# Performance work log

Hardware: AMD Instinct MI355X
Metric: run time of the kernel (lower is better)

Reference implementation:

```python
import jax, jax.numpy as jnp
import numpy as np

WIN = (7, 7)
N_TOK = WIN[0] * WIN[1]          # 49
DIM = 512
HEADS = 16
B_WIN = 2048                     # num_windows * batch
NW = 64                          # windows per image (mask leading dim)


def _relative_position_index():
    # Mirrors the torch __init__ coords computation.
    coords = np.stack(np.meshgrid(np.arange(WIN[0]), np.arange(WIN[1]), indexing='ij'))  # [2,Wh,Ww]
    flat = coords.reshape(2, -1)                                   # [2, N]
    rel = flat[:, :, None] - flat[:, None, :]                      # [2, N, N]
    rel = rel.transpose(1, 2, 0).astype(np.int32)                  # [N, N, 2]
    rel[:, :, 0] += WIN[0] - 1
    rel[:, :, 1] += WIN[1] - 1
    rel[:, :, 0] *= 2 * WIN[1] - 1
    return jnp.asarray(rel.sum(-1), dtype=jnp.int32)               # [N, N]


def setup_inputs() -> dict:
    key = jax.random.key(0)
    ks = jax.random.split(key, 7)
    x = jax.random.normal(ks[0], (B_WIN, N_TOK, DIM), jnp.float32)
    w_qkv = jax.random.normal(ks[1], (3 * DIM, DIM), jnp.float32) * 0.02
    b_qkv = jax.random.normal(ks[2], (3 * DIM,), jnp.float32) * 0.02
    w_proj = jax.random.normal(ks[3], (DIM, DIM), jnp.float32) * 0.02
    b_proj = jax.random.normal(ks[4], (DIM,), jnp.float32) * 0.02
    bias_table = jax.random.normal(ks[5], ((2 * WIN[0] - 1) * (2 * WIN[1] - 1), HEADS), jnp.float32) * 0.02
    rel_index = _relative_position_index()
    # shift-window mask: 0 for allowed, -100 for masked (Swin convention)
    mask = jnp.where(jax.random.bernoulli(ks[6], 0.1, (NW, N_TOK, N_TOK)), -100.0, 0.0).astype(jnp.float32)
    return {"x": x, "w_qkv": w_qkv, "b_qkv": b_qkv, "w_proj": w_proj,
            "b_proj": b_proj, "bias_table": bias_table, "rel_index": rel_index, "mask": mask}


def reference(x, w_qkv, b_qkv, w_proj, b_proj, bias_table, rel_index, mask):
    B_, N, C = x.shape
    H = HEADS
    hd = C // H
    scale = hd ** -0.5
    # qkv projection: [B, N, 3, H, hd] -> q,k,v each [B, H, N, hd]
    qkv = (jnp.einsum('bnc,oc->bno', x, w_qkv) + b_qkv)
    qkv = qkv.reshape(B_, N, 3, H, hd).transpose(2, 0, 3, 1, 4)
    q, k, v = qkv[0], qkv[1], qkv[2]
    attn = jnp.einsum('bhnd,bhmd->bhnm', q * scale, k)             # [B, H, N, N]
    # relative position bias gather: [N*N] -> [N, N, H] -> [H, N, N]
    rpb = bias_table[rel_index.reshape(-1)].reshape(N, N, H).transpose(2, 0, 1)
    attn = attn + rpb[None]
    nW = mask.shape[0]
    attn = attn.reshape(B_ // nW, nW, H, N, N) + mask[None, :, None]
    attn = attn.reshape(B_, H, N, N)
    attn = jax.nn.softmax(attn, axis=-1)
    out = jnp.einsum('bhnm,bhmd->bhnd', attn, v)                   # [B, H, N, hd]
    out = out.transpose(0, 2, 1, 3).reshape(B_, N, C)
    out = jnp.einsum('bnc,oc->bno', out, w_proj) + b_proj
    return out
```

## Files before the change

### kernel.cpp

```cpp
#include <hip/hip_runtime.h>
#include <stdint.h>

typedef unsigned short u16;
typedef unsigned int u32;
typedef unsigned long long u64;
typedef __attribute__((ext_vector_type(4))) u16 u16x4;
typedef __attribute__((ext_vector_type(8))) u16 u16x8;
typedef __attribute__((ext_vector_type(2))) u32 u32x2;
typedef __attribute__((ext_vector_type(8))) short bf16x8;
typedef __attribute__((ext_vector_type(4))) float f32x4;

#define DEVFN __device__ __forceinline__

DEVFN u16 f2bf(float f) {
  union { float f; u32 u; } x; x.f = f;
  u32 u = x.u;
  return (u16)((u + 0x7fffu + ((u >> 16) & 1u)) >> 16);
}
DEVFN float bf2f(u16 v) {
  union { u32 u; float f; } x; x.u = ((u32)v) << 16;
  return x.f;
}

__global__ void cvt_kernel(const float* __restrict__ in, u16* __restrict__ out, int n4) {
  const int stride = gridDim.x * blockDim.x;
  for (int i = blockIdx.x * blockDim.x + threadIdx.x; i < n4; i += stride) {
    float4 v = reinterpret_cast<const float4*>(in)[i];
    u16x4 o;
    o.x = f2bf(v.x); o.y = f2bf(v.y); o.z = f2bf(v.z); o.w = f2bf(v.w);
    reinterpret_cast<u16x4*>(out)[i] = o;
  }
}

__global__ void pbb_kernel(const float* __restrict__ bt, const int* __restrict__ ri,
                           u16* __restrict__ pbb) {
  const int h = blockIdx.x;
  for (int t = threadIdx.x; t < 4096; t += 256) {
    const int i = t >> 6, j = t & 63;
    float v = 0.f;
    if (i < 49 && j < 49) v = bt[ri[i * 49 + j] * 16 + h];
    pbb[h * 4096 + t] = f2bf(v);
  }
}

__global__ void mbits_kernel(const float* __restrict__ mask, u64* __restrict__ mb) {
  const int w = blockIdx.x;
  const int i = threadIdx.x;
  u64 m = ~0ull << 49;
  if (i < 49) {
    for (int j = 0; j < 49; ++j)
      if (mask[w * 2401 + i * 49 + j] < -1.0f) m |= 1ull << j;
  } else {
    m = ~0ull;
  }
  mb[w * 64 + i] = m;
}

#define WAIT_LGKM0 asm volatile("s_waitcnt lgkmcnt(0)" ::: "memory")
#define WAIT_LGKM8 asm volatile("s_waitcnt lgkmcnt(8)" ::: "memory")
#define WAIT_VM2   asm volatile("s_waitcnt vmcnt(2)" ::: "memory")
#define WAIT_VM0   asm volatile("s_waitcnt vmcnt(0)" ::: "memory")
#define SCHEDB     __builtin_amdgcn_sched_barrier(0)
#define BARRIER    __builtin_amdgcn_s_barrier()
#define MFMA(a, b, c) __builtin_amdgcn_mfma_f32_16x16x32_bf16(a, b, c, 0, 0, 0)

template <int MODE, int NTILES, int MCHUNK>
__global__ __launch_bounds__(512) void gemm_kernel(
    const u16* __restrict__ A, const u16* __restrict__ Bt,
    const float* __restrict__ bias, void* __restrict__ Out, int ldo) {
  extern __shared__ u16 smem[];
  const int tid = threadIdx.x;
  const int lane = tid & 63;
  const int wid = tid >> 6;
  const int bid = blockIdx.x;
  const int xcd = bid & 7;
  const int slot = bid >> 3;
  const int m0 = (xcd * MCHUNK + slot / NTILES) * 256;
  const int n0 = (slot % NTILES) * 256;
  const int wr = wid >> 2, wc = wid & 3;
  const int l15 = lane & 15, lg = lane >> 4;
  const int rg0 = tid >> 3;
  const int sl0 = tid & 7;

  f32x4 acc[8][4] = {};

#define STAGE_RAW(kt_, hp_)                                                    \
  {                                                                            \
    const u16* srcp_ = ((hp_) < 2)                                             \
        ? (A + (size_t)(m0 + ((hp_) & 1) * 128) * 512)                         \
        : (Bt + (size_t)(n0 + ((hp_) & 1) * 128) * 512);                       \
    u16* dst_ = smem + ((kt_) & 1) * 32768 + (hp_) * 8192;                     \
    _Pragma("unroll") for (int i_ = 0; i_ < 2; ++i_) {                         \
      const int rg_ = i_ * 64 + rg0;                                           \
      const int kc_ = sl0 ^ (rg_ & 7);                                         \
      const u16* g_ = srcp_ + (size_t)rg_ * 512 + (kt_) * 64 + kc_ * 8;        \
      __builtin_amdgcn_global_load_lds(                                        \
          (const __attribute__((address_space(1))) void*)g_,                   \
          (__attribute__((address_space(3))) void*)(dst_ + i_ * 4096 + wid * 512), \
          16, 0, 0);                                                           \
    }                                                                          \
  }

#define STG(g_)                                                                \
  if ((g_) >= 3 && (g_) < 27) {                                                \
    const int s_ = (g_) - 3;                                                   \
    STAGE_RAW(2 + s_ / 4, s_ & 3);                                             \
  }

#define RDA(dst, mi_, ks_)                                                     \
  {                                                                            \
    const int row_ = wr * 128 + (mi_) * 16 + l15;                              \
    dst = *reinterpret_cast<const bf16x8*>(                                    \
        smem + cb + row_ * 64 + ((((ks_) * 4 + lg) ^ (row_ & 7)) << 3));       \
  }
#define RDB(dst, ni_, ks_)                                                     \
  {                                                                            \
    const int row_ = wc * 64 + (ni_) * 16 + l15;                               \
    dst = *reinterpret_cast<const bf16x8*>(                                    \
        smem + cb + 16384 + row_ * 64 + ((((ks_) * 4 + lg) ^ (row_ & 7)) << 3)); \
  }

#pragma unroll
  for (int hp = 0; hp < 4; ++hp) STAGE_RAW(0, hp);
#pragma unroll
  for (int hp = 0; hp < 4; ++hp) STAGE_RAW(1, hp);
  WAIT_VM0; SCHEDB;
  BARRIER; SCHEDB;

#pragma unroll
  for (int kt = 0; kt < 8; ++kt) {
    const int cb = (kt & 1) * 32768;
    const int g0 = kt * 4;
    bf16x8 a0[4][2], a1[4][2], b0[2][2], b1[2][2];

#pragma unroll
    for (int mi = 0; mi < 4; ++mi) { RDA(a0[mi][0], mi, 0); RDA(a0[mi][1], mi, 1); }
#pragma unroll
    for (int ni = 0; ni < 2; ++ni) { RDB(b0[ni][0], ni, 0); RDB(b0[ni][1], ni, 1); }
    STG(g0 + 0);
    WAIT_LGKM8; SCHEDB;
    BARRIER;
    WAIT_LGKM0; SCHEDB;
    __builtin_amdgcn_s_setprio(1);
#pragma unroll
    for (int mi = 0; mi < 4; ++mi)
#pragma unroll
      for (int ni = 0; ni < 2; ++ni)
#pragma unroll
        for (int ks = 0; ks < 2; ++ks)
          acc[mi][ni] = MFMA(a0[mi][ks], b0[ni][ks], acc[mi][ni]);
    __builtin_amdgcn_s_setprio(0); SCHEDB;
    BARRIER; SCHEDB;

#pragma unroll
    for (int ni = 0; ni < 2; ++ni) { RDB(b1[ni][0], ni + 2, 0); RDB(b1[ni][1], ni + 2, 1); }
    STG(g0 + 1);
    BARRIER;
    WAIT_LGKM0; SCHEDB;
    __builtin_amdgcn_s_setprio(1);
#pragma unroll
    for (int mi = 0; mi < 4; ++mi)
#pragma unroll
      for (int ni = 0; ni < 2; ++ni)
#pragma unroll
        for (int ks = 0; ks < 2; ++ks)
          acc[mi][ni + 2] = MFMA(a0[mi][ks], b1[ni][ks], acc[mi][ni + 2]);
    __builtin_amdgcn_s_setprio(0); SCHEDB;
    BARRIER; SCHEDB;

#pragma unroll
    for (int mi = 0; mi < 4; ++mi) { RDA(a1[mi][0], mi + 4, 0); RDA(a1[mi][1], mi + 4, 1); }
    STG(g0 + 2);
    BARRIER;
    WAIT_LGKM0; SCHEDB;
    __builtin_amdgcn_s_setprio(1);
#pragma unroll
    for (int mi = 0; mi < 4; ++mi)
#pragma unroll
      for (int ni = 0; ni < 2; ++ni)
#pragma unroll
        for (int ks = 0; ks < 2; ++ks)
          acc[mi + 4][ni + 2] = MFMA(a1[mi][ks], b1[ni][ks], acc[mi + 4][ni + 2]);
    __builtin_amdgcn_s_setprio(0); SCHEDB;
    BARRIER; SCHEDB;

    STG(g0 + 3);
    BARRIER; SCHEDB;
    __builtin_amdgcn_s_setprio(1);
#pragma unroll
    for (int mi = 0; mi < 4; ++mi)
#pragma unroll
      for (int ni = 0; ni < 2; ++ni)
#pragma unroll
        for (int ks = 0; ks < 2; ++ks)
          acc[mi + 4][ni] = MFMA(a1[mi][ks], b0[ni][ks], acc[mi + 4][ni]);
    __builtin_amdgcn_s_setprio(0); SCHEDB;
    if (g0 + 3 == 27) { WAIT_VM0; }
    else if (g0 + 3 < 27) { WAIT_VM2; }
    SCHEDB;
    BARRIER; SCHEDB;
  }
#undef STAGE_RAW
#undef STG
#undef RDA
#undef RDB

#pragma unroll
  for (int mi = 0; mi < 8; ++mi) {
#pragma unroll
    for (int ni = 0; ni < 4; ++ni) {
      const int col = n0 + wc * 64 + ni * 16 + l15;
      const float bv = bias[col];
      const int rbase = m0 + wr * 128 + mi * 16 + lg * 4;
#pragma unroll
      for (int r = 0; r < 4; ++r) {
        const float v = acc[mi][ni][r] + bv;
        if (MODE == 0) {
          ((u16*)Out)[(size_t)(rbase + r) * ldo + col] = f2bf(v);
        } else {
          ((float*)Out)[(size_t)(rbase + r) * ldo + col] = v;
        }
      }
    }
  }
}

__global__ __launch_bounds__(256) void attn_kernel(
    const u16* __restrict__ qkv, const u16* __restrict__ pbb,
    const u64* __restrict__ mbits, u16* __restrict__ attn_out) {
  const int w = threadIdx.x >> 6;
  const int lane = threadIdx.x & 63;
  const int b = blockIdx.x >> 2;
  const int h = ((blockIdx.x & 3) << 2) | w;
  const int l15 = lane & 15, lg = lane >> 4;
  const int lg4 = lg * 4;

  __shared__ u16 sVT[4][32][72];
  u16 (*vt)[72] = sVT[w];

  for (int i = lane; i < 1152; i += 64) ((u32*)vt)[i] = 0;

  const size_t rowbase = (size_t)b * (49 * 1536) + h * 32;

  for (int c = lane; c < 196; c += 64) {
    const int n = c >> 2, dg = c & 3;
    u16x8 vv = *reinterpret_cast<const u16x8*>(qkv + rowbase + (size_t)n * 1536 + 1024 + dg * 8);
    const int pin = ((n >> 5) << 5) | ((((n >> 2) & 3)) << 3) | (((n >> 4) & 1) << 2) | (n & 3);
#pragma unroll
    for (int j = 0; j < 8; ++j) vt[dg * 8 + j][pin] = vv[j];
  }

  bf16x8 aq[4], bk[4];
#pragma unroll
  for (int t = 0; t < 4; ++t) {
    const int i = t * 16 + l15;
    const int r = i < 49 ? i : 48;
    const size_t ro = rowbase + (size_t)r * 1536 + lg * 8;
    aq[t] = *reinterpret_cast<const bf16x8*>(qkv + ro);
    bk[t] = *reinterpret_cast<const bf16x8*>(qkv + ro + 512);
  }

  const u64* mwb = mbits + ((b & 63) << 6);
  u64 mb[4];
#pragma unroll
  for (int qt = 0; qt < 4; ++qt) mb[qt] = mwb[qt * 16 + l15];

  bf16x8 bv[2][2];
#pragma unroll
  for (int ni = 0; ni < 2; ++ni)
#pragma unroll
    for (int ks = 0; ks < 2; ++ks)
      bv[ni][ks] = *reinterpret_cast<const bf16x8*>(&vt[ni * 16 + l15][ks * 32 + lg * 8]);

  const float scale = 0.17677669529663687f;
  const u16* pbh = pbb + (h << 12);
  const size_t obase = (size_t)b * 49 * 512 + h * 32;

#pragma unroll
  for (int qt = 0; qt < 4; ++qt) {
    f32x4 sT[4] = {};
#pragma unroll
    for (int kt = 0; kt < 4; ++kt)
      sT[kt] = __builtin_amdgcn_mfma_f32_16x16x32_bf16(bk[kt], aq[qt], sT[kt], 0, 0, 0);

    const int i = qt * 16 + l15;
    const u16* pr = pbh + i * 64 + lg4;
    float v[4][4];
    float mx = -3e38f;
#pragma unroll
    for (int kt = 0; kt < 4; ++kt) {
      u16x4 pv = *reinterpret_cast<const u16x4*>(pr + kt * 16);
      const u32 nib = (u32)(mb[qt] >> (kt * 16 + lg4)) & 0xFu;
#pragma unroll
      for (int r = 0; r < 4; ++r) {
        float val = fmaf(sT[kt][r], scale, bf2f(pv[r]));
        if (nib & (1u << r)) val -= 100.f;
        if (kt == 3 && (lg4 + r) >= 1) val = -1e30f;
        v[kt][r] = val;
        mx = fmaxf(mx, val);
      }
    }
    mx = fmaxf(mx, __shfl_xor(mx, 16));
    mx = fmaxf(mx, __shfl_xor(mx, 32));
    float sum = 0.f;
#pragma unroll
    for (int kt = 0; kt < 4; ++kt)
#pragma unroll
      for (int r = 0; r < 4; ++r) {
        const float e = __expf(v[kt][r] - mx);
        v[kt][r] = e;
        sum += e;
      }
    sum += __shfl_xor(sum, 16);
    sum += __shfl_xor(sum, 32);
    const float rinv = 1.0f / sum;

    bf16x8 ap[2];
#pragma unroll
    for (int ks = 0; ks < 2; ++ks) {
      u32 w0 = (u32)f2bf(v[2 * ks][0] * rinv) | ((u32)f2bf(v[2 * ks][1] * rinv) << 16);
      u32 w1 = (u32)f2bf(v[2 * ks][2] * rinv) | ((u32)f2bf(v[2 * ks][3] * rinv) << 16);
      u32 w2 = (u32)f2bf(v[2 * ks + 1][0] * rinv) | ((u32)f2bf(v[2 * ks + 1][1] * rinv) << 16);
      u32 w3 = (u32)f2bf(v[2 * ks + 1][2] * rinv) | ((u32)f2bf(v[2 * ks + 1][3] * rinv) << 16);
      union { u32 u[4]; bf16x8 b; } pk;
      pk.u[0] = w0; pk.u[1] = w1; pk.u[2] = w2; pk.u[3] = w3;
      ap[ks] = pk.b;
    }

    f32x4 o[2] = {};
#pragma unroll
    for (int ks = 0; ks < 2; ++ks)
#pragma unroll
      for (int ni = 0; ni < 2; ++ni)
        o[ni] = __builtin_amdgcn_mfma_f32_16x16x32_bf16(ap[ks], bv[ni][ks], o[ni], 0, 0, 0);

#pragma unroll
    for (int r = 0; r < 4; ++r) {
      const int iq = qt * 16 + lg4 + r;
      if (iq < 49) {
#pragma unroll
        for (int ni = 0; ni < 2; ++ni)
          attn_out[obase + (size_t)iq * 512 + ni * 16 + l15] = f2bf(o[ni][r]);
      }
    }
  }
}

extern "C" void kernel_launch(void* const* d_in, const int* in_sizes, int n_in,
                              void* d_out, int out_size, void* d_ws, size_t ws_size,
                              hipStream_t stream) {
  (void)in_sizes; (void)n_in; (void)out_size; (void)ws_size;
  const float* x          = (const float*)d_in[0];
  const float* w_qkv      = (const float*)d_in[1];
  const float* b_qkv      = (const float*)d_in[2];
  const float* w_proj     = (const float*)d_in[3];
  const float* b_proj     = (const float*)d_in[4];
  const float* bias_table = (const float*)d_in[5];
  const int*   rel_index  = (const int*)d_in[6];
  const float* mask       = (const float*)d_in[7];

  u16* ws     = (u16*)d_ws;
  u16* xbf    = ws;
  u16* qkv    = ws + 51380224;
  u16* wqkvb  = qkv + 154140672;
  u16* wprojb = wqkvb + 786432;
  u16* pbb    = wprojb + 262144;
  u64* mbits  = (u64*)(pbb + 65536);

  (void)hipFuncSetAttribute((const void*)gemm_kernel<0, 6, 49>,
                            hipFuncAttributeMaxDynamicSharedMemorySize, 131072);
  (void)hipFuncSetAttribute((const void*)gemm_kernel<1, 2, 49>,
                            hipFuncAttributeMaxDynamicSharedMemorySize, 131072);

  cvt_kernel<<<2048, 256, 0, stream>>>(x, xbf, 51380224 / 4);
  cvt_kernel<<<192, 256, 0, stream>>>(w_qkv, wqkvb, 786432 / 4);
  cvt_kernel<<<64, 256, 0, stream>>>(w_proj, wprojb, 262144 / 4);
  pbb_kernel<<<16, 256, 0, stream>>>(bias_table, rel_index, pbb);
  mbits_kernel<<<64, 64, 0, stream>>>(mask, mbits);

  gemm_kernel<0, 6, 49><<<2352, 512, 131072, stream>>>(xbf, wqkvb, b_qkv, qkv, 1536);
  attn_kernel<<<8192, 256, 0, stream>>>(qkv, pbb, mbits, xbf);
  gemm_kernel<1, 2, 49><<<784, 512, 131072, stream>>>(xbf, wprojb, b_proj, d_out, 512);
}
```

Baseline: 505.4 us.

## Reschedule GEMM prefetch stages, use nontemporal stores, and XCD-swizzle attention blocks

```diff
diff --git a/kernel.cpp b/kernel.cpp
--- a/kernel.cpp
+++ b/kernel.cpp
@@ -58,7 +58,7 @@
 
 #define WAIT_LGKM0 asm volatile("s_waitcnt lgkmcnt(0)" ::: "memory")
 #define WAIT_LGKM8 asm volatile("s_waitcnt lgkmcnt(8)" ::: "memory")
-#define WAIT_VM2   asm volatile("s_waitcnt vmcnt(2)" ::: "memory")
+#define WAIT_VM4   asm volatile("s_waitcnt vmcnt(4)" ::: "memory")
 #define WAIT_VM0   asm volatile("s_waitcnt vmcnt(0)" ::: "memory")
 #define SCHEDB     __builtin_amdgcn_sched_barrier(0)
 #define BARRIER    __builtin_amdgcn_s_barrier()
@@ -101,12 +101,6 @@
     }                                                                          \
   }
 
-#define STG(g_)                                                                \
-  if ((g_) >= 3 && (g_) < 27) {                                                \
-    const int s_ = (g_) - 3;                                                   \
-    STAGE_RAW(2 + s_ / 4, s_ & 3);                                             \
-  }
-
 #define RDA(dst, mi_, ks_)                                                     \
   {                                                                            \
     const int row_ = wr * 128 + (mi_) * 16 + l15;                              \
@@ -130,14 +124,13 @@
 #pragma unroll
   for (int kt = 0; kt < 8; ++kt) {
     const int cb = (kt & 1) * 32768;
-    const int g0 = kt * 4;
     bf16x8 a0[4][2], a1[4][2], b0[2][2], b1[2][2];
 
 #pragma unroll
     for (int mi = 0; mi < 4; ++mi) { RDA(a0[mi][0], mi, 0); RDA(a0[mi][1], mi, 1); }
 #pragma unroll
     for (int ni = 0; ni < 2; ++ni) { RDB(b0[ni][0], ni, 0); RDB(b0[ni][1], ni, 1); }
-    STG(g0 + 0);
+    if (kt >= 1 && kt <= 6) STAGE_RAW(kt + 1, 2);
     WAIT_LGKM8; SCHEDB;
     BARRIER;
     WAIT_LGKM0; SCHEDB;
@@ -154,7 +147,7 @@
 
 #pragma unroll
     for (int ni = 0; ni < 2; ++ni) { RDB(b1[ni][0], ni + 2, 0); RDB(b1[ni][1], ni + 2, 1); }
-    STG(g0 + 1);
+    if (kt >= 1 && kt <= 6) STAGE_RAW(kt + 1, 3);
     BARRIER;
     WAIT_LGKM0; SCHEDB;
     __builtin_amdgcn_s_setprio(1);
@@ -170,7 +163,6 @@
 
 #pragma unroll
     for (int mi = 0; mi < 4; ++mi) { RDA(a1[mi][0], mi + 4, 0); RDA(a1[mi][1], mi + 4, 1); }
-    STG(g0 + 2);
     BARRIER;
     WAIT_LGKM0; SCHEDB;
     __builtin_amdgcn_s_setprio(1);
@@ -184,7 +176,7 @@
     __builtin_amdgcn_s_setprio(0); SCHEDB;
     BARRIER; SCHEDB;
 
-    STG(g0 + 3);
+    if (kt <= 5) { STAGE_RAW(kt + 2, 0); STAGE_RAW(kt + 2, 1); }
     BARRIER; SCHEDB;
     __builtin_amdgcn_s_setprio(1);
 #pragma unroll
@@ -195,13 +187,12 @@
         for (int ks = 0; ks < 2; ++ks)
           acc[mi + 4][ni] = MFMA(a1[mi][ks], b0[ni][ks], acc[mi + 4][ni]);
     __builtin_amdgcn_s_setprio(0); SCHEDB;
-    if (g0 + 3 == 27) { WAIT_VM0; }
-    else if (g0 + 3 < 27) { WAIT_VM2; }
+    if (kt <= 5) { WAIT_VM4; }
+    else if (kt == 6) { WAIT_VM0; }
     SCHEDB;
-    BARRIER; SCHEDB;
+    if (kt < 7) { BARRIER; SCHEDB; }
   }
 #undef STAGE_RAW
-#undef STG
 #undef RDA
 #undef RDB
 
@@ -216,9 +207,9 @@
       for (int r = 0; r < 4; ++r) {
         const float v = acc[mi][ni][r] + bv;
         if (MODE == 0) {
-          ((u16*)Out)[(size_t)(rbase + r) * ldo + col] = f2bf(v);
+          __builtin_nontemporal_store(f2bf(v), &((u16*)Out)[(size_t)(rbase + r) * ldo + col]);
         } else {
-          ((float*)Out)[(size_t)(rbase + r) * ldo + col] = v;
+          __builtin_nontemporal_store(v, &((float*)Out)[(size_t)(rbase + r) * ldo + col]);
         }
       }
     }
@@ -230,8 +221,10 @@
     const u64* __restrict__ mbits, u16* __restrict__ attn_out) {
   const int w = threadIdx.x >> 6;
   const int lane = threadIdx.x & 63;
-  const int b = blockIdx.x >> 2;
-  const int h = ((blockIdx.x & 3) << 2) | w;
+  const int xcd = blockIdx.x & 7;
+  const int rest = blockIdx.x >> 3;
+  const int b = xcd * 256 + (rest >> 2);
+  const int h = ((rest & 3) << 2) | w;
   const int l15 = lane & 15, lg = lane >> 4;
   const int lg4 = lg * 4;
 
```

Measured after the change: 590.8 us. +16.9%, slower.
